# Performance work log

Measured on AMD Instinct MI355X. Metric: run time of the kernel, lower is better.

## Reference

```python
import jax, jax.numpy as jnp
import numpy as np

TAU = 0.1

def setup_inputs() -> dict:
    key = jax.random.key(0)
    kZ, k1, k2 = jax.random.split(key, 3)
    N, D = 8192, 128
    scale = 1.0 / np.sqrt(D)
    return {
        "Z": jax.random.normal(kZ, (N, D), dtype=jnp.float32),
        "W1": jax.random.normal(k1, (D, D), dtype=jnp.float32) * scale,
        "b1": jnp.zeros((D,), dtype=jnp.float32),
        "W2": jax.random.normal(k2, (D, D), dtype=jnp.float32) * scale,
        "b2": jnp.zeros((D,), dtype=jnp.float32),
    }

def reference(Z, W1, b1, W2, b2):
    # DiffusivityTransform: 2-layer MLP with ReLU (torch Linear: x @ W.T + b;
    # here W1/W2 are stored already transposed as [in, out])
    t = jax.nn.relu(Z @ W1 + b1) @ W2 + b2          # [N, D]
    sim = t @ t.T                                     # [N, N]
    S = jax.nn.softmax(sim, axis=1)                   # row-stochastic [N, N]
    Z_prop = S @ Z                                    # [N, D]
    return Z + TAU * (Z_prop - Z)
```

## Files before the change

### kernel.cpp

```cpp
#include <hip/hip_runtime.h>

typedef _Float16 half_t;
typedef _Float16 hx8 __attribute__((ext_vector_type(8)));
typedef _Float16 hx4 __attribute__((ext_vector_type(4)));
typedef float fx4 __attribute__((ext_vector_type(4)));

#define LOG2E 1.44269504088896f
#define TAU 0.1f
#define NSPLIT 8

__global__ __launch_bounds__(256) void wtrans_kernel(
    const float* __restrict__ W1, const float* __restrict__ W2,
    half_t* __restrict__ W1t, half_t* __restrict__ W2t)
{
  __shared__ float tile[32*132];
  const int bx = blockIdx.x;
  const float* W = (bx & 4) ? W2 : W1;
  half_t* Wt = (bx & 4) ? W2t : W1t;
  const int i0 = (bx & 3) * 32;
  const int tid = threadIdx.x;
  const int r = tid >> 3, cb = tid & 7;
#pragma unroll
  for (int it=0; it<4; ++it) {
    int c4 = cb*4 + it*32;
    *(fx4*)(&tile[r*132 + c4]) = *(const fx4*)(W + (size_t)(i0+r)*128 + c4);
  }
  __syncthreads();
  const int o = tid >> 1, ih = (tid & 1)*16;
  hx8 v0, v1;
#pragma unroll
  for (int u=0;u<8;++u) v0[u] = (half_t)tile[(ih+u)*132 + o];
#pragma unroll
  for (int u=0;u<8;++u) v1[u] = (half_t)tile[(ih+8+u)*132 + o];
  *(hx8*)(Wt + (size_t)o*128 + i0 + ih)     = v0;
  *(hx8*)(Wt + (size_t)o*128 + i0 + ih + 8) = v1;
}

__global__ __launch_bounds__(256) void mlpz_kernel(
    const float* __restrict__ Z, const half_t* __restrict__ W1t,
    const float* __restrict__ b1, const half_t* __restrict__ W2t,
    const float* __restrict__ b2, half_t* __restrict__ T,
    half_t* __restrict__ Zth)
{
  __shared__ float Ztile[64*132];
  __shared__ half_t Hs[4][16*136];
  const int tid = threadIdx.x;
  const int w = tid >> 6, lane = tid & 63;
  const int q = lane >> 4, c = lane & 15;
  const int rb = blockIdx.x*64;
  const int wrow = rb + w*16;

#pragma unroll
  for (int i=0;i<8;++i) {
    int fid = i*256 + tid;
    int r = fid >> 5, c4 = (fid & 31)*4;
    *(fx4*)(&Ztile[r*132 + c4]) = *(const fx4*)(Z + (size_t)(rb + r)*128 + c4);
  }
  __syncthreads();

  {
    const int d = tid >> 1, n0 = (tid & 1)*32;
#pragma unroll
    for (int i=0;i<4;++i) {
      hx8 hv;
#pragma unroll
      for (int u=0;u<8;++u) hv[u] = (half_t)Ztile[(n0 + i*8 + u)*132 + d];
      *(hx8*)(Zth + (size_t)d*8192 + rb + n0 + i*8) = hv;
    }
  }

  hx8 zb[4];
#pragma unroll
  for (int ks=0;ks<4;++ks) {
    fx4 a = *(const fx4*)(&Ztile[(w*16 + c)*132 + ks*32 + q*8]);
    fx4 b = *(const fx4*)(&Ztile[(w*16 + c)*132 + ks*32 + q*8 + 4]);
#pragma unroll
    for (int u=0;u<4;++u) { zb[ks][u] = (half_t)a[u]; zb[ks][4+u] = (half_t)b[u]; }
  }

  fx4 acc[8];
#pragma unroll
  for (int mt=0;mt<8;++mt) acc[mt] = (fx4){0.f,0.f,0.f,0.f};
#pragma unroll
  for (int mt=0;mt<8;++mt)
#pragma unroll
    for (int ks=0;ks<4;++ks) {
      hx8 aw = *(const hx8*)(W1t + (size_t)(mt*16 + c)*128 + ks*32 + q*8);
      acc[mt] = __builtin_amdgcn_mfma_f32_16x16x32_f16(aw, zb[ks], acc[mt], 0,0,0);
    }
#pragma unroll
  for (int mt=0;mt<8;++mt) {
    fx4 bias = *(const fx4*)(b1 + mt*16 + 4*q);
    hx4 hv;
#pragma unroll
    for (int i=0;i<4;++i) {
      float h = acc[mt][i] + bias[i];
      hv[i] = (half_t)(h > 0.f ? h : 0.f);
    }
    *(hx4*)(&Hs[w][c*136 + mt*16 + 4*q]) = hv;
  }

  hx8 hb[4];
#pragma unroll
  for (int ks=0;ks<4;++ks) hb[ks] = *(const hx8*)(&Hs[w][c*136 + ks*32 + q*8]);
#pragma unroll
  for (int mt=0;mt<8;++mt) acc[mt] = (fx4){0.f,0.f,0.f,0.f};
#pragma unroll
  for (int mt=0;mt<8;++mt)
#pragma unroll
    for (int ks=0;ks<4;++ks) {
      hx8 aw = *(const hx8*)(W2t + (size_t)(mt*16 + c)*128 + ks*32 + q*8);
      acc[mt] = __builtin_amdgcn_mfma_f32_16x16x32_f16(aw, hb[ks], acc[mt], 0,0,0);
    }
#pragma unroll
  for (int mt=0;mt<8;++mt) {
    fx4 bias = *(const fx4*)(b2 + mt*16 + 4*q);
    hx4 tv;
#pragma unroll
    for (int i=0;i<4;++i) tv[i] = (half_t)(acc[mt][i] + bias[i]);
    *(hx4*)(T + (size_t)(wrow + c)*128 + mt*16 + 4*q) = tv;
  }
}

__global__ __launch_bounds__(256,2) void flash_kernel(
    const half_t* __restrict__ T, const half_t* __restrict__ Zt,
    half_t* __restrict__ Pacc, float* __restrict__ Pm, float* __restrict__ Pl)
{
  __shared__ half_t Tbuf[2][16*512];
  __shared__ half_t Zbuf[2][16*512];
  const int tid = threadIdx.x;
  const int w = tid >> 6, lane = tid & 63;
  const int q = lane >> 4, c = lane & 15;
  const int bx = blockIdx.x;
  const int qb = bx >> 3, kh = bx & 7;
  const int wrow = qb*128 + w*32;
  const int sw = (c & 7) * 8;

  hx8 bq[2][4];
#pragma unroll
  for (int nt=0;nt<2;++nt)
#pragma unroll
    for (int ks=0;ks<4;++ks)
      bq[nt][ks] = *(const hx8*)(T + (size_t)(wrow + nt*16 + c)*128 + ks*32 + q*8);

  fx4 oacc[8][2];
#pragma unroll
  for (int mtd=0;mtd<8;++mtd)
#pragma unroll
    for (int nt=0;nt<2;++nt) oacc[mtd][nt] = (fx4){0.f,0.f,0.f,0.f};
  float m_run[2] = {-1e30f,-1e30f};
  float l_run[2] = {0.f,0.f};

  const int kbase = kh*1024;

  auto issue_loads = [&](int kt0, int b) {
    if (w < 2) {
#pragma unroll
      for (int i=0;i<8;++i) {
        int f = w*8 + i, mt = f >> 2, ks = f & 3;
        const half_t* gp = T + (size_t)(kt0 + mt*16 + c)*128 + ks*32 + q*8;
        half_t* lp = &Tbuf[b][f*512 + lane*8];
        __builtin_amdgcn_global_load_lds(
            (const __attribute__((address_space(1))) void*)gp,
            (__attribute__((address_space(3))) void*)lp, 16, 0, 0);
      }
    } else {
#pragma unroll
      for (int i=0;i<8;++i) {
        int f2 = (w-2)*8 + i, mtd = f2 >> 1, ks2 = f2 & 1;
        const half_t* gp = Zt + (size_t)(mtd*16 + c)*8192 + kt0 + ks2*32 + q*8;
        half_t* lp = &Zbuf[b][f2*512 + lane*8];
        __builtin_amdgcn_global_load_lds(
            (const __attribute__((address_space(1))) void*)gp,
            (__attribute__((address_space(3))) void*)lp, 16, 0, 0);
      }
    }
  };

  issue_loads(kbase, 0);

  for (int t=0;t<16;++t) {
    const int cur = t & 1;
    __syncthreads();
    if (t < 15) issue_loads(kbase + (t+1)*64, cur ^ 1);
    half_t* Tcur = Tbuf[cur];
    half_t* Zcur = Zbuf[cur];
    half_t* Psw  = &Tbuf[cur][w*2048];

    fx4 sacc[4][2];
#pragma unroll
    for (int mt=0;mt<4;++mt)
#pragma unroll
      for (int nt=0;nt<2;++nt) sacc[mt][nt] = (fx4){0.f,0.f,0.f,0.f};
#pragma unroll
    for (int ks=0;ks<4;++ks)
#pragma unroll
      for (int mt=0;mt<4;++mt) {
        hx8 ak = *(const hx8*)(&Tcur[(mt*4+ks)*512 + lane*8]);
        sacc[mt][0] = __builtin_amdgcn_mfma_f32_16x16x32_f16(ak, bq[0][ks], sacc[mt][0], 0,0,0);
        sacc[mt][1] = __builtin_amdgcn_mfma_f32_16x16x32_f16(ak, bq[1][ks], sacc[mt][1], 0,0,0);
      }

    hx4 pk[2][4];
#pragma unroll
    for (int nt=0;nt<2;++nt) {
      float mx = -1e30f;
#pragma unroll
      for (int mt=0;mt<4;++mt)
#pragma unroll
        for (int i=0;i<4;++i) mx = fmaxf(mx, sacc[mt][nt][i]);
      mx = fmaxf(mx, __shfl_xor(mx, 16, 64));
      mx = fmaxf(mx, __shfl_xor(mx, 32, 64));
      float mnew = fmaxf(m_run[nt], mx);
      float alpha = __builtin_amdgcn_exp2f((m_run[nt]-mnew)*LOG2E);
      m_run[nt] = mnew;
      float nb = mnew*LOG2E;
      float rs = 0.f;
#pragma unroll
      for (int mt=0;mt<4;++mt) {
#pragma unroll
        for (int i=0;i<4;++i) {
          float p = __builtin_amdgcn_exp2f(sacc[mt][nt][i]*LOG2E - nb);
          rs += p;
          pk[nt][mt][i] = (half_t)p;
        }
      }
      rs += __shfl_xor(rs, 16, 64);
      rs += __shfl_xor(rs, 32, 64);
      l_run[nt] = l_run[nt]*alpha + rs;
      if (__any(alpha != 1.0f)) {
#pragma unroll
        for (int mtd=0;mtd<8;++mtd)
#pragma unroll
          for (int i=0;i<4;++i) oacc[mtd][nt][i] *= alpha;
      }
    }

    __syncthreads();
#pragma unroll
    for (int nt=0;nt<2;++nt)
#pragma unroll
      for (int mt=0;mt<4;++mt)
        *(hx4*)(&Psw[(nt*16 + c)*64 + ((mt*16 + 4*q) ^ sw)]) = pk[nt][mt];

#pragma unroll
    for (int ks2=0;ks2<2;++ks2) {
      hx8 bp0 = *(const hx8*)(&Psw[(c     )*64 + ((ks2*32 + q*8) ^ sw)]);
      hx8 bp1 = *(const hx8*)(&Psw[(16 + c)*64 + ((ks2*32 + q*8) ^ sw)]);
#pragma unroll
      for (int mtd=0;mtd<8;++mtd) {
        hx8 az = *(const hx8*)(&Zcur[(mtd*2+ks2)*512 + lane*8]);
        oacc[mtd][0] = __builtin_amdgcn_mfma_f32_16x16x32_f16(az, bp0, oacc[mtd][0], 0,0,0);
        oacc[mtd][1] = __builtin_amdgcn_mfma_f32_16x16x32_f16(az, bp1, oacc[mtd][1], 0,0,0);
      }
    }
  }

#pragma unroll
  for (int nt=0;nt<2;++nt) {
    float inv = 1.0f / l_run[nt];
    const size_t rowg = (size_t)(bx*128 + w*32 + nt*16 + c);
#pragma unroll
    for (int mtd=0;mtd<8;++mtd) {
      hx4 ov;
#pragma unroll
      for (int i=0;i<4;++i) ov[i] = (half_t)(oacc[mtd][nt][i]*inv);
      *(hx4*)(Pacc + rowg*128 + mtd*16 + 4*q) = ov;
    }
    if (q == 0) {
      Pm[rowg] = m_run[nt];
      Pl[rowg] = l_run[nt];
    }
  }
}

__global__ __launch_bounds__(256) void merge_kernel(
    const float* __restrict__ Z, const half_t* __restrict__ Pacc,
    const float* __restrict__ Pm, const float* __restrict__ Pl,
    float* __restrict__ out)
{
  const int th = blockIdx.x*256 + threadIdx.x;
  const int r = th >> 5, cg = th & 31;
  const int qb = r >> 7, rr = r & 127;
  float mk[NSPLIT], lk[NSPLIT];
  float M = -1e30f;
#pragma unroll
  for (int k=0;k<NSPLIT;++k) {
    int p = qb*NSPLIT + k;
    mk[k] = Pm[p*128 + rr];
    lk[k] = Pl[p*128 + rr];
    M = fmaxf(M, mk[k]);
  }
  float L = 0.f, wk[NSPLIT];
#pragma unroll
  for (int k=0;k<NSPLIT;++k) { wk[k] = lk[k]*__builtin_amdgcn_exp2f((mk[k]-M)*LOG2E); L += wk[k]; }
  float o0=0.f,o1=0.f,o2=0.f,o3=0.f;
#pragma unroll
  for (int k=0;k<NSPLIT;++k) {
    int p = qb*NSPLIT + k;
    hx4 v = *(const hx4*)(Pacc + ((size_t)p*128 + rr)*128 + cg*4);
    o0 += wk[k]*(float)v[0]; o1 += wk[k]*(float)v[1];
    o2 += wk[k]*(float)v[2]; o3 += wk[k]*(float)v[3];
  }
  float invL = 1.0f / L;
  fx4 zv = *(const fx4*)(Z + (size_t)r*128 + cg*4);
  fx4 res;
  res[0] = (1.f-TAU)*zv[0] + TAU*o0*invL;
  res[1] = (1.f-TAU)*zv[1] + TAU*o1*invL;
  res[2] = (1.f-TAU)*zv[2] + TAU*o2*invL;
  res[3] = (1.f-TAU)*zv[3] + TAU*o3*invL;
  *(fx4*)(out + (size_t)r*128 + cg*4) = res;
}

extern "C" void kernel_launch(void* const* d_in, const int* in_sizes, int n_in,
                              void* d_out, int out_size, void* d_ws, size_t ws_size,
                              hipStream_t stream) {
  const float* Z  = (const float*)d_in[0];
  const float* W1 = (const float*)d_in[1];
  const float* b1 = (const float*)d_in[2];
  const float* W2 = (const float*)d_in[3];
  const float* b2 = (const float*)d_in[4];
  float* out = (float*)d_out;

  char* ws = (char*)d_ws;
  const size_t NBLK = 64 * NSPLIT;
  half_t* Thi  = (half_t*)(ws);
  half_t* Zth  = (half_t*)(ws + (size_t)2*1024*1024);
  half_t* Pacc = (half_t*)(ws + (size_t)4*1024*1024);
  float*  Pm   = (float*)(ws + (size_t)4*1024*1024 + NBLK*128*128*2);
  float*  Pl   = Pm + NBLK*128;
  half_t* W1t  = (half_t*)(ws + (size_t)4*1024*1024 + NBLK*128*128*2 + 2*NBLK*128*4);
  half_t* W2t  = W1t + 128*128;

  hipLaunchKernelGGL(wtrans_kernel, dim3(8),    dim3(256), 0, stream, W1, W2, W1t, W2t);
  hipLaunchKernelGGL(mlpz_kernel,   dim3(128),  dim3(256), 0, stream, Z, W1t, b1, W2t, b2, Thi, Zth);
  hipLaunchKernelGGL(flash_kernel,  dim3(NBLK), dim3(256), 0, stream, Thi, Zth, Pacc, Pm, Pl);
  hipLaunchKernelGGL(merge_kernel,  dim3(1024), dim3(256), 0, stream, Z, Pacc, Pm, Pl, out);
}
```

Measured before the change: 134.6 us.

## Drop weight transpose kernel, move prefetch after barrier, always rescale accumulators

```diff
diff --git a/kernel.cpp b/kernel.cpp
--- a/kernel.cpp
+++ b/kernel.cpp
@@ -9,36 +9,9 @@
 #define TAU 0.1f
 #define NSPLIT 8
 
-__global__ __launch_bounds__(256) void wtrans_kernel(
-    const float* __restrict__ W1, const float* __restrict__ W2,
-    half_t* __restrict__ W1t, half_t* __restrict__ W2t)
-{
-  __shared__ float tile[32*132];
-  const int bx = blockIdx.x;
-  const float* W = (bx & 4) ? W2 : W1;
-  half_t* Wt = (bx & 4) ? W2t : W1t;
-  const int i0 = (bx & 3) * 32;
-  const int tid = threadIdx.x;
-  const int r = tid >> 3, cb = tid & 7;
-#pragma unroll
-  for (int it=0; it<4; ++it) {
-    int c4 = cb*4 + it*32;
-    *(fx4*)(&tile[r*132 + c4]) = *(const fx4*)(W + (size_t)(i0+r)*128 + c4);
-  }
-  __syncthreads();
-  const int o = tid >> 1, ih = (tid & 1)*16;
-  hx8 v0, v1;
-#pragma unroll
-  for (int u=0;u<8;++u) v0[u] = (half_t)tile[(ih+u)*132 + o];
-#pragma unroll
-  for (int u=0;u<8;++u) v1[u] = (half_t)tile[(ih+8+u)*132 + o];
-  *(hx8*)(Wt + (size_t)o*128 + i0 + ih)     = v0;
-  *(hx8*)(Wt + (size_t)o*128 + i0 + ih + 8) = v1;
-}
-
 __global__ __launch_bounds__(256) void mlpz_kernel(
-    const float* __restrict__ Z, const half_t* __restrict__ W1t,
-    const float* __restrict__ b1, const half_t* __restrict__ W2t,
+    const float* __restrict__ Z, const float* __restrict__ W1,
+    const float* __restrict__ b1, const float* __restrict__ W2,
     const float* __restrict__ b2, half_t* __restrict__ T,
     half_t* __restrict__ Zth)
 {
@@ -85,7 +58,10 @@
   for (int mt=0;mt<8;++mt)
 #pragma unroll
     for (int ks=0;ks<4;++ks) {
-      hx8 aw = *(const hx8*)(W1t + (size_t)(mt*16 + c)*128 + ks*32 + q*8);
+      hx8 aw;
+#pragma unroll
+      for (int j=0;j<8;++j)
+        aw[j] = (half_t)W1[(size_t)(ks*32 + q*8 + j)*128 + mt*16 + c];
       acc[mt] = __builtin_amdgcn_mfma_f32_16x16x32_f16(aw, zb[ks], acc[mt], 0,0,0);
     }
 #pragma unroll
@@ -109,7 +85,10 @@
   for (int mt=0;mt<8;++mt)
 #pragma unroll
     for (int ks=0;ks<4;++ks) {
-      hx8 aw = *(const hx8*)(W2t + (size_t)(mt*16 + c)*128 + ks*32 + q*8);
+      hx8 aw;
+#pragma unroll
+      for (int j=0;j<8;++j)
+        aw[j] = (half_t)W2[(size_t)(ks*32 + q*8 + j)*128 + mt*16 + c];
       acc[mt] = __builtin_amdgcn_mfma_f32_16x16x32_f16(aw, hb[ks], acc[mt], 0,0,0);
     }
 #pragma unroll
@@ -182,7 +161,6 @@
   for (int t=0;t<16;++t) {
     const int cur = t & 1;
     __syncthreads();
-    if (t < 15) issue_loads(kbase + (t+1)*64, cur ^ 1);
     half_t* Tcur = Tbuf[cur];
     half_t* Zcur = Zbuf[cur];
     half_t* Psw  = &Tbuf[cur][w*2048];
@@ -228,15 +206,15 @@
       rs += __shfl_xor(rs, 16, 64);
       rs += __shfl_xor(rs, 32, 64);
       l_run[nt] = l_run[nt]*alpha + rs;
-      if (__any(alpha != 1.0f)) {
-#pragma unroll
-        for (int mtd=0;mtd<8;++mtd)
-#pragma unroll
-          for (int i=0;i<4;++i) oacc[mtd][nt][i] *= alpha;
-      }
+#pragma unroll
+      for (int mtd=0;mtd<8;++mtd)
+#pragma unroll
+        for (int i=0;i<4;++i) oacc[mtd][nt][i] *= alpha;
     }
 
     __syncthreads();
+    if (t < 15) issue_loads(kbase + (t+1)*64, cur ^ 1);
+
 #pragma unroll
     for (int nt=0;nt<2;++nt)
 #pragma unroll
@@ -329,11 +307,8 @@
   half_t* Pacc = (half_t*)(ws + (size_t)4*1024*1024);
   float*  Pm   = (float*)(ws + (size_t)4*1024*1024 + NBLK*128*128*2);
   float*  Pl   = Pm + NBLK*128;
-  half_t* W1t  = (half_t*)(ws + (size_t)4*1024*1024 + NBLK*128*128*2 + 2*NBLK*128*4);
-  half_t* W2t  = W1t + 128*128;
-
-  hipLaunchKernelGGL(wtrans_kernel, dim3(8),    dim3(256), 0, stream, W1, W2, W1t, W2t);
-  hipLaunchKernelGGL(mlpz_kernel,   dim3(128),  dim3(256), 0, stream, Z, W1t, b1, W2t, b2, Thi, Zth);
-  hipLaunchKernelGGL(flash_kernel,  dim3(NBLK), dim3(256), 0, stream, Thi, Zth, Pacc, Pm, Pl);
-  hipLaunchKernelGGL(merge_kernel,  dim3(1024), dim3(256), 0, stream, Z, Pacc, Pm, Pl, out);
+
+  hipLaunchKernelGGL(mlpz_kernel,  dim3(128),  dim3(256), 0, stream, Z, W1, b1, W2, b2, Thi, Zth);
+  hipLaunchKernelGGL(flash_kernel, dim3(NBLK), dim3(256), 0, stream, Thi, Zth, Pacc, Pm, Pl);
+  hipLaunchKernelGGL(merge_kernel, dim3(1024), dim3(256), 0, stream, Z, Pacc, Pm, Pl, out);
 }
```

After: 131.0 us. 2.7% less time.
